# Performance work log

Measured on AMD Instinct MI355X. Metric: run time of the kernel, lower is better.

Reference implementation:

```python
import jax, jax.numpy as jnp
import numpy as np
from jax import lax

B, N = 65536, 126  # batch, atoms (N % 3 == 0)


def _normalize(x):
    # matches torch.nn.functional.normalize(x, dim=-1): x / max(||x||, 1e-12)
    n = jnp.sqrt(jnp.sum(x * x, axis=-1, keepdims=True))
    return x / jnp.maximum(n, 1e-12)


def setup_inputs() -> dict:
    key = jax.random.key(0)
    k1, k2 = jax.random.split(key)
    angles = jax.random.normal(k1, (B, 2 * N), dtype=jnp.float32)
    prev_three = jax.random.normal(k2, (B, 3, 3), dtype=jnp.float32)
    return {"angles": angles, "prev_three": prev_three}


def _forward(angles, prev_three):
    Bb, L = angles.shape
    Nn = L // 2
    # chunk last dim into 2 halves, cat along dim 1, reshape, transpose -> (B, N, 2)
    ang = jnp.concatenate(jnp.split(angles, 2, axis=-1), axis=1)
    ang = ang.reshape(Bb, 2, Nn).transpose(0, 2, 1)
    sin_t = ang[..., 0]
    cos_t = ang[..., 1]
    n_t = jnp.sqrt(sin_t ** 2 + cos_t ** 2 + 1e-8)
    sin_t = sin_t / n_t
    cos_t = cos_t / n_t
    alpha = jnp.tile(jnp.array([2.028, 2.124, 1.941], dtype=angles.dtype), Nn // 3)  # (N,)
    bond = jnp.tile(jnp.array([1.329, 1.458, 1.523], dtype=angles.dtype), Nn // 3)   # (N,)
    sin_a = jnp.sin(alpha)[None, :]
    cos_a = jnp.broadcast_to(jnp.cos(alpha)[None, :], (Bb, Nn))
    rotation = jnp.stack([cos_a, sin_a * cos_t, -sin_a * sin_t], axis=2) * bond[None, :, None]  # (B,N,3)

    a0 = prev_three[:, 0, :]
    b0 = prev_three[:, 1, :]
    c0 = prev_three[:, 2, :]

    def step(carry, rot):
        # rot: (B, 3) for one atom
        a, b, c = carry
        bc = _normalize(b - c + 1e-8)
        n = _normalize(jnp.cross(b - a, bc) + 1e-8)
        m1 = jnp.cross(n, bc)
        d = c + rot[:, 0:1] * bc + rot[:, 1:2] * m1 + rot[:, 2:3] * n  # (B,3)
        return (b, c, d), d

    _, res = lax.scan(step, (a0, b0, c0), rotation.transpose(1, 0, 2))  # res: (N,B,3)
    return res.transpose(1, 0, 2)  # (B,N,3)


def reference(angles, prev_three):
    return _forward(angles, prev_three)
```

## Files before the change

### kernel.cpp

```cpp
#include <hip/hip_runtime.h>
#include <math.h>

#define NRES 126
#define SEGS 14
#define SLEN 9
#define RPB  32
#define TPB  (RPB * SEGS)

__device__ __forceinline__ float grsq(float x) {
    return __builtin_amdgcn_rsqf(fmaxf(x, 1e-24f));
}

__global__ __launch_bounds__(TPB, 4) void DihedralToCartesian_kernel(
    const float* __restrict__ angles,
    const float* __restrict__ prev,
    float* __restrict__ out,
    int nrows)
{
    __shared__ float E[TPB][13];
    __shared__ float F0[RPB][13];

    if (blockIdx.x * RPB >= nrows) return;

    const int t   = threadIdx.x;
    const int s   = t % SEGS;
    const int rl  = t / SEGS;
    const int row = blockIdx.x * RPB + rl;

    const float* ga = angles + (size_t)row * 252 + s * SLEN;
    float sn[SLEN], cs[SLEN];
    #pragma unroll
    for (int j = 0; j < SLEN; ++j) { sn[j] = ga[j]; cs[j] = ga[126 + j]; }

    if (s == 0) {
        const float* pr = prev + (size_t)row * 9;
        float a0=pr[0],a1=pr[1],a2=pr[2];
        float b0=pr[3],b1=pr[4],b2=pr[5];
        float c0=pr[6],c1=pr[7],c2=pr[8];
        float ux=b0-c0+1e-8f, uy=b1-c1+1e-8f, uz=b2-c2+1e-8f;
        float ru=grsq(ux*ux+uy*uy+uz*uz); ux*=ru; uy*=ru; uz*=ru;
        float vx=b0-a0, vy=b1-a1, vz=b2-a2;
        float nx=vy*uz-vz*uy+1e-8f, ny=vz*ux-vx*uz+1e-8f, nz=vx*uy-vy*ux+1e-8f;
        float rn=grsq(nx*nx+ny*ny+nz*nz); nx*=rn; ny*=rn; nz*=rn;
        float mx=ny*uz-nz*uy, my=nz*ux-nx*uz, mz=nx*uy-ny*ux;
        float* f = F0[rl];
        f[0]=ux; f[1]=mx; f[2]=nx;
        f[3]=uy; f[4]=my; f[5]=ny;
        f[6]=uz; f[7]=mz; f[8]=nz;
        f[9]=c0; f[10]=c1; f[11]=c2;
    }

    const float ca0=cosf(2.028f), sa0=sinf(2.028f), bc0=1.329f*ca0, bs0=1.329f*sa0;
    const float ca1=cosf(2.124f), sa1=sinf(2.124f), bc1=1.458f*ca1, bs1=1.458f*sa1;
    const float ca2=cosf(1.941f), sa2=sinf(1.941f), bc2=1.523f*ca2, bs2=1.523f*sa2;

    float r0,r1,r2,r3,r4,r5,r6,r7,r8, tx,ty,tz;
    float p[3 * SLEN];

    #pragma unroll
    for (int j = 0; j < SLEN; ++j) {
        const int ph = j % 3;
        const float ca  = (ph==0)?ca0:(ph==1)?ca1:ca2;
        const float sa  = (ph==0)?sa0:(ph==1)?sa1:sa2;
        const float bca = (ph==0)?bc0:(ph==1)?bc1:bc2;
        const float bsa = (ph==0)?bs0:(ph==1)?bs1:bs2;

        float rr = __builtin_amdgcn_rsqf(sn[j]*sn[j] + cs[j]*cs[j] + 1e-8f);
        float st = sn[j]*rr, ct = cs[j]*rr;
        float m10=-sa*ct, m11=-ca*ct, m20=sa*st, m21=ca*st;
        float tl1=bsa*ct, tl2=-bsa*st;

        if (j == 0) {
            r0=-ca;  r1=sa;   r2=0.f;
            r3=m10;  r4=m11;  r5=st;
            r6=m20;  r7=m21;  r8=ct;
            tx=bca;  ty=tl1;  tz=tl2;
        } else {
            float n0 = r0*(-ca) + r1*m10 + r2*m20;
            float n1 = r0*sa    + r1*m11 + r2*m21;
            float n2 =            r1*st  + r2*ct;
            float n3 = r3*(-ca) + r4*m10 + r5*m20;
            float n4 = r3*sa    + r4*m11 + r5*m21;
            float n5 =            r4*st  + r5*ct;
            float n6 = r6*(-ca) + r7*m10 + r8*m20;
            float n7 = r6*sa    + r7*m11 + r8*m21;
            float n8 =            r7*st  + r8*ct;
            float q0 = tx + r0*bca + r1*tl1 + r2*tl2;
            float q1 = ty + r3*bca + r4*tl1 + r5*tl2;
            float q2 = tz + r6*bca + r7*tl1 + r8*tl2;
            r0=n0; r1=n1; r2=n2; r3=n3; r4=n4; r5=n5; r6=n6; r7=n7; r8=n8;
            tx=q0; ty=q1; tz=q2;
        }
        p[3*j+0]=tx; p[3*j+1]=ty; p[3*j+2]=tz;
    }

    {
        float* e = E[t];
        e[0]=r0; e[1]=r1; e[2]=r2; e[3]=r3; e[4]=r4; e[5]=r5;
        e[6]=r6; e[7]=r7; e[8]=r8; e[9]=tx; e[10]=ty; e[11]=tz;
    }
    __syncthreads();

    #pragma unroll
    for (int l = 0; l < 4; ++l) {
        const int d = 1 << l;
        const bool act = (s >= d);
        float A[12];
        if (act) {
            const float* a = E[t - d];
            #pragma unroll
            for (int w = 0; w < 12; ++w) A[w] = a[w];
            float n0 = A[0]*r0 + A[1]*r3 + A[2]*r6;
            float n1 = A[0]*r1 + A[1]*r4 + A[2]*r7;
            float n2 = A[0]*r2 + A[1]*r5 + A[2]*r8;
            float n3 = A[3]*r0 + A[4]*r3 + A[5]*r6;
            float n4 = A[3]*r1 + A[4]*r4 + A[5]*r7;
            float n5 = A[3]*r2 + A[4]*r5 + A[5]*r8;
            float n6 = A[6]*r0 + A[7]*r3 + A[8]*r6;
            float n7 = A[6]*r1 + A[7]*r4 + A[8]*r7;
            float n8 = A[6]*r2 + A[7]*r5 + A[8]*r8;
            float q0 = A[9]  + A[0]*tx + A[1]*ty + A[2]*tz;
            float q1 = A[10] + A[3]*tx + A[4]*ty + A[5]*tz;
            float q2 = A[11] + A[6]*tx + A[7]*ty + A[8]*tz;
            r0=n0; r1=n1; r2=n2; r3=n3; r4=n4; r5=n5; r6=n6; r7=n7; r8=n8;
            tx=q0; ty=q1; tz=q2;
        }
        __syncthreads();
        if (act) {
            float* e = E[t];
            e[0]=r0; e[1]=r1; e[2]=r2; e[3]=r3; e[4]=r4; e[5]=r5;
            e[6]=r6; e[7]=r7; e[8]=r8; e[9]=tx; e[10]=ty; e[11]=tz;
        }
        __syncthreads();
    }

    float P0,P1,P2,P3,P4,P5,P6,P7,P8, Pt0,Pt1,Pt2;
    {
        const float* f = F0[rl];
        if (s == 0) {
            P0=f[0]; P1=f[1]; P2=f[2];
            P3=f[3]; P4=f[4]; P5=f[5];
            P6=f[6]; P7=f[7]; P8=f[8];
            Pt0=f[9]; Pt1=f[10]; Pt2=f[11];
        } else {
            const float* b = E[t - 1];
            P0 = f[0]*b[0] + f[1]*b[3] + f[2]*b[6];
            P1 = f[0]*b[1] + f[1]*b[4] + f[2]*b[7];
            P2 = f[0]*b[2] + f[1]*b[5] + f[2]*b[8];
            P3 = f[3]*b[0] + f[4]*b[3] + f[5]*b[6];
            P4 = f[3]*b[1] + f[4]*b[4] + f[5]*b[7];
            P5 = f[3]*b[2] + f[4]*b[5] + f[5]*b[8];
            P6 = f[6]*b[0] + f[7]*b[3] + f[8]*b[6];
            P7 = f[6]*b[1] + f[7]*b[4] + f[8]*b[7];
            P8 = f[6]*b[2] + f[7]*b[5] + f[8]*b[8];
            Pt0 = f[9]  + f[0]*b[9] + f[1]*b[10] + f[2]*b[11];
            Pt1 = f[10] + f[3]*b[9] + f[4]*b[10] + f[5]*b[11];
            Pt2 = f[11] + f[6]*b[9] + f[7]*b[10] + f[8]*b[11];
        }
    }

    float* go = out + (size_t)row * 378 + s * 27;
    #pragma unroll
    for (int j = 0; j < SLEN; ++j) {
        float px=p[3*j], py=p[3*j+1], pz=p[3*j+2];
        go[3*j+0] = Pt0 + P0*px + P1*py + P2*pz;
        go[3*j+1] = Pt1 + P3*px + P4*py + P5*pz;
        go[3*j+2] = Pt2 + P6*px + P7*py + P8*pz;
    }
}

extern "C" void kernel_launch(void* const* d_in, const int* in_sizes, int n_in,
                              void* d_out, int out_size, void* d_ws, size_t ws_size,
                              hipStream_t stream)
{
    const float* angles = (const float*)d_in[0];
    const float* prev   = (const float*)d_in[1];
    float*       out    = (float*)d_out;

    int nrows = in_sizes[1] / 9;
    int grid  = (nrows + RPB - 1) / RPB;

    DihedralToCartesian_kernel<<<grid, TPB, 0, stream>>>(angles, prev, out, nrows);
}
```

Before: 174.4 us.

## Stage input and output through shared memory for coalesced global access

Angles are loaded cooperatively into a shared buffer with fully coalesced strided accesses, and outputs are staged in shared memory and then written out coalesced, replacing per-thread strided 9/27-float accesses. To save registers, the per-atom positions array is dropped and the local chain is recomputed in a second pass starting from the prefix transform. Occupancy is raised via launch bounds (5 blocks/SM). The cost is a larger shared buffer (about 48KB), extra syncs, and duplicated arithmetic.

```diff
diff --git a/kernel.cpp b/kernel.cpp
--- a/kernel.cpp
+++ b/kernel.cpp
@@ -1,39 +1,40 @@
 #include <hip/hip_runtime.h>
 #include <math.h>
 
-#define NRES 126
 #define SEGS 14
 #define SLEN 9
 #define RPB  32
 #define TPB  (RPB * SEGS)
+#define INF  (TPB * 18)
+#define STF  (TPB * 27)
 
 __device__ __forceinline__ float grsq(float x) {
     return __builtin_amdgcn_rsqf(fmaxf(x, 1e-24f));
 }
 
-__global__ __launch_bounds__(TPB, 4) void DihedralToCartesian_kernel(
+__global__ __launch_bounds__(TPB, 5) void DihedralToCartesian_kernel(
     const float* __restrict__ angles,
     const float* __restrict__ prev,
     float* __restrict__ out,
     int nrows)
 {
-    __shared__ float E[TPB][13];
+    __shared__ float buf[STF];
     __shared__ float F0[RPB][13];
 
     if (blockIdx.x * RPB >= nrows) return;
 
-    const int t   = threadIdx.x;
-    const int s   = t % SEGS;
-    const int rl  = t / SEGS;
-    const int row = blockIdx.x * RPB + rl;
-
-    const float* ga = angles + (size_t)row * 252 + s * SLEN;
-    float sn[SLEN], cs[SLEN];
-    #pragma unroll
-    for (int j = 0; j < SLEN; ++j) { sn[j] = ga[j]; cs[j] = ga[126 + j]; }
+    const int t  = threadIdx.x;
+    const int s  = t % SEGS;
+    const int rl = t / SEGS;
+    const size_t gin  = (size_t)blockIdx.x * (RPB * 252);
+    const size_t gout = (size_t)blockIdx.x * (RPB * 378);
+
+    #pragma unroll
+    for (int i = 0; i < 18; ++i)
+        buf[i * TPB + t] = angles[gin + i * TPB + t];
 
     if (s == 0) {
-        const float* pr = prev + (size_t)row * 9;
+        const float* pr = prev + (size_t)(blockIdx.x * RPB + rl) * 9;
         float a0=pr[0],a1=pr[1],a2=pr[2];
         float b0=pr[3],b1=pr[4],b2=pr[5];
         float c0=pr[6],c1=pr[7],c2=pr[8];
@@ -50,13 +51,22 @@
         f[9]=c0; f[10]=c1; f[11]=c2;
     }
 
+    __syncthreads();
+
+    float sn[SLEN], cs[SLEN];
+    {
+        const float* myin = buf + rl * 252 + s * SLEN;
+        #pragma unroll
+        for (int j = 0; j < SLEN; ++j) { sn[j] = myin[j]; cs[j] = myin[126 + j]; }
+    }
+
+    __syncthreads();
+
     const float ca0=cosf(2.028f), sa0=sinf(2.028f), bc0=1.329f*ca0, bs0=1.329f*sa0;
     const float ca1=cosf(2.124f), sa1=sinf(2.124f), bc1=1.458f*ca1, bs1=1.458f*sa1;
     const float ca2=cosf(1.941f), sa2=sinf(1.941f), bc2=1.523f*ca2, bs2=1.523f*sa2;
 
     float r0,r1,r2,r3,r4,r5,r6,r7,r8, tx,ty,tz;
-    float p[3 * SLEN];
-
     #pragma unroll
     for (int j = 0; j < SLEN; ++j) {
         const int ph = j % 3;
@@ -76,6 +86,9 @@
             r6=m20;  r7=m21;  r8=ct;
             tx=bca;  ty=tl1;  tz=tl2;
         } else {
+            float q0 = tx + r0*bca + r1*tl1 + r2*tl2;
+            float q1 = ty + r3*bca + r4*tl1 + r5*tl2;
+            float q2 = tz + r6*bca + r7*tl1 + r8*tl2;
             float n0 = r0*(-ca) + r1*m10 + r2*m20;
             float n1 = r0*sa    + r1*m11 + r2*m21;
             float n2 =            r1*st  + r2*ct;
@@ -85,17 +98,13 @@
             float n6 = r6*(-ca) + r7*m10 + r8*m20;
             float n7 = r6*sa    + r7*m11 + r8*m21;
             float n8 =            r7*st  + r8*ct;
-            float q0 = tx + r0*bca + r1*tl1 + r2*tl2;
-            float q1 = ty + r3*bca + r4*tl1 + r5*tl2;
-            float q2 = tz + r6*bca + r7*tl1 + r8*tl2;
             r0=n0; r1=n1; r2=n2; r3=n3; r4=n4; r5=n5; r6=n6; r7=n7; r8=n8;
             tx=q0; ty=q1; tz=q2;
         }
-        p[3*j+0]=tx; p[3*j+1]=ty; p[3*j+2]=tz;
-    }
-
-    {
-        float* e = E[t];
+    }
+
+    {
+        float* e = buf + t * 13;
         e[0]=r0; e[1]=r1; e[2]=r2; e[3]=r3; e[4]=r4; e[5]=r5;
         e[6]=r6; e[7]=r7; e[8]=r8; e[9]=tx; e[10]=ty; e[11]=tz;
     }
@@ -105,9 +114,9 @@
     for (int l = 0; l < 4; ++l) {
         const int d = 1 << l;
         const bool act = (s >= d);
-        float A[12];
         if (act) {
-            const float* a = E[t - d];
+            const float* a = buf + (t - d) * 13;
+            float A[12];
             #pragma unroll
             for (int w = 0; w < 12; ++w) A[w] = a[w];
             float n0 = A[0]*r0 + A[1]*r3 + A[2]*r6;
@@ -127,7 +136,7 @@
         }
         __syncthreads();
         if (act) {
-            float* e = E[t];
+            float* e = buf + t * 13;
             e[0]=r0; e[1]=r1; e[2]=r2; e[3]=r3; e[4]=r4; e[5]=r5;
             e[6]=r6; e[7]=r7; e[8]=r8; e[9]=tx; e[10]=ty; e[11]=tz;
         }
@@ -143,7 +152,7 @@
             P6=f[6]; P7=f[7]; P8=f[8];
             Pt0=f[9]; Pt1=f[10]; Pt2=f[11];
         } else {
-            const float* b = E[t - 1];
+            const float* b = buf + (t - 1) * 13;
             P0 = f[0]*b[0] + f[1]*b[3] + f[2]*b[6];
             P1 = f[0]*b[1] + f[1]*b[4] + f[2]*b[7];
             P2 = f[0]*b[2] + f[1]*b[5] + f[2]*b[8];
@@ -159,14 +168,47 @@
         }
     }
 
-    float* go = out + (size_t)row * 378 + s * 27;
-    #pragma unroll
-    for (int j = 0; j < SLEN; ++j) {
-        float px=p[3*j], py=p[3*j+1], pz=p[3*j+2];
-        go[3*j+0] = Pt0 + P0*px + P1*py + P2*pz;
-        go[3*j+1] = Pt1 + P3*px + P4*py + P5*pz;
-        go[3*j+2] = Pt2 + P6*px + P7*py + P8*pz;
-    }
+    __syncthreads();
+
+    {
+        float* st = buf + rl * 378 + s * 27;
+        #pragma unroll
+        for (int j = 0; j < SLEN; ++j) {
+            const int ph = j % 3;
+            const float ca  = (ph==0)?ca0:(ph==1)?ca1:ca2;
+            const float sa  = (ph==0)?sa0:(ph==1)?sa1:sa2;
+            const float bca = (ph==0)?bc0:(ph==1)?bc1:bc2;
+            const float bsa = (ph==0)?bs0:(ph==1)?bs1:bs2;
+
+            float rr = __builtin_amdgcn_rsqf(sn[j]*sn[j] + cs[j]*cs[j] + 1e-8f);
+            float st_ = sn[j]*rr, ct = cs[j]*rr;
+            float m10=-sa*ct, m11=-ca*ct, m20=sa*st_, m21=ca*st_;
+            float tl1=bsa*ct, tl2=-bsa*st_;
+
+            float q0 = Pt0 + P0*bca + P1*tl1 + P2*tl2;
+            float q1 = Pt1 + P3*bca + P4*tl1 + P5*tl2;
+            float q2 = Pt2 + P6*bca + P7*tl1 + P8*tl2;
+            float n0 = P0*(-ca) + P1*m10 + P2*m20;
+            float n1 = P0*sa    + P1*m11 + P2*m21;
+            float n2 =            P1*st_ + P2*ct;
+            float n3 = P3*(-ca) + P4*m10 + P5*m20;
+            float n4 = P3*sa    + P4*m11 + P5*m21;
+            float n5 =            P4*st_ + P5*ct;
+            float n6 = P6*(-ca) + P7*m10 + P8*m20;
+            float n7 = P6*sa    + P7*m11 + P8*m21;
+            float n8 =            P7*st_ + P8*ct;
+            P0=n0; P1=n1; P2=n2; P3=n3; P4=n4; P5=n5; P6=n6; P7=n7; P8=n8;
+            Pt0=q0; Pt1=q1; Pt2=q2;
+
+            st[3*j+0] = q0; st[3*j+1] = q1; st[3*j+2] = q2;
+        }
+    }
+
+    __syncthreads();
+
+    #pragma unroll
+    for (int i = 0; i < 27; ++i)
+        out[gout + i * TPB + t] = buf[i * TPB + t];
 }
 
 extern "C" void kernel_launch(void* const* d_in, const int* in_sizes, int n_in,
```

Result: slower. 209.4 us (+20.1%).
